# Optimization experiments

Measured on AMD Instinct MI355X. Metric: run time of the kernel, lower is better.

## Reference

```python
import jax, jax.numpy as jnp
import numpy as np

H = 768   # config.hidden_size
B = 1024  # batch
S = 256   # attention context length
C1, C2, C3 = 202, 183, 11  # num_class for crit, law, time


def setup_inputs() -> dict:
    key = jax.random.key(0)
    ks = jax.random.split(key, 18)
    sd = 1.0 / np.sqrt(H)
    def u(k, shape):
        return jax.random.uniform(k, shape, jnp.float32, -sd, sd)
    return {
        "x": jax.random.normal(ks[0], (B, H), jnp.float32),
        "attn": jax.random.normal(ks[1], (B, S, H), jnp.float32),
        # 3 LSTMCells (tasks crit, law, time), stacked
        "Wih": u(ks[2], (3, 4 * H, H)),
        "Whh": u(ks[3], (3, 4 * H, H)),
        "bih": u(ks[4], (3, 4 * H)),
        "bhh": u(ks[5], (3, 4 * H)),
        # edge (2->3) hidden/cell state Linear (only edge whose FC is reached)
        "hfc_W": u(ks[6], (H, H)), "hfc_b": u(ks[7], (H,)),
        "cfc_W": u(ks[8], (H, H)), "cfc_b": u(ks[9], (H,)),
        # midfc per task
        "midfc_W": u(ks[10], (3, H, H)), "midfc_b": u(ks[11], (3, H)),
        # outfc per task (distinct class counts)
        "out1_W": u(ks[12], (C1, H)), "out1_b": u(ks[13], (C1,)),
        "out2_W": u(ks[14], (C2, H)), "out2_b": u(ks[15], (C2,)),
        "out3_W": u(ks[16], (C3, H)), "out3_b": u(ks[17], (C3,)),
    }


def _lstm_cell(x, h, c, Wih, Whh, bih, bhh):
    # torch nn.LSTMCell: gate order i, f, g, o
    gates = x @ Wih.T + bih + h @ Whh.T + bhh
    i, f, g, o = jnp.split(gates, 4, axis=-1)
    c_new = jax.nn.sigmoid(f) * c + jax.nn.sigmoid(i) * jnp.tanh(g)
    h_new = jax.nn.sigmoid(o) * jnp.tanh(c_new)
    return h_new, c_new


def _attend(h, attn):
    # Attention: ratio = softmax(bmm(attn, h)); result = bmm(attn^T, ratio)
    w = jax.nn.softmax(jnp.einsum('bsh,bh->bs', attn, h), axis=1)
    return jnp.einsum('bsh,bs->bh', attn, w)


def _head(h, mW, mb, oW, ob):
    # more_fc=True: outfc(relu(midfc(h)))
    return jax.nn.relu(h @ mW.T + mb) @ oW.T + ob


def reference(x, attn, Wih, Whh, bih, bhh, hfc_W, hfc_b, cfc_W, cfc_b,
              midfc_W, midfc_b, out1_W, out1_b, out2_W, out2_b, out3_W, out3_b):
    # graph "[(1 2),(1 3),(2 3)]": edges 1->2, 1->3, 2->3; initial hidden_list all zero.
    z = jnp.zeros_like(x)
    # task 1 (crit): runs on zero state; first-touch sets hidden[2]=hidden[3]=(h1,c1)
    h1, c1 = _lstm_cell(x, z, z, Wih[0], Whh[0], bih[0], bhh[0])
    # task 2 (law): state = (h1, c1)
    h2, c2 = _lstm_cell(x, h1, c1, Wih[1], Whh[1], bih[1], bhh[1])
    # edge 2->3 applies the per-edge Linear and accumulates into hidden[3]
    hp3 = h1 + h2 @ hfc_W.T + hfc_b
    cp3 = c1 + c2 @ cfc_W.T + cfc_b
    # task 3 (time)
    h3, c3 = _lstm_cell(x, hp3, cp3, Wih[2], Whh[2], bih[2], bhh[2])
    # attention over encoder context, per task head
    a1 = _attend(h1, attn)
    a2 = _attend(h2, attn)
    a3 = _attend(h3, attn)
    o1 = _head(a1, midfc_W[0], midfc_b[0], out1_W, out1_b)
    o2 = _head(a2, midfc_W[1], midfc_b[1], out2_W, out2_b)
    o3 = _head(a3, midfc_W[2], midfc_b[2], out3_W, out3_b)
    return (o1, o2, o3)
```

## Files before the change

### kernel.cpp

```cpp
#include <hip/hip_runtime.h>


typedef unsigned short u16;
typedef _Float16       f16x8 __attribute__((ext_vector_type(8)));
typedef float          f32x4 __attribute__((ext_vector_type(4)));

#define SWZ(r) ((((r) + ((r) >> 2))) & 3)
#define VMCNT(N) asm volatile("s_waitcnt vmcnt(" #N ")" ::: "memory")
#define KBAR()  do { __builtin_amdgcn_s_barrier(); __builtin_amdgcn_sched_barrier(0); } while (0)

__device__ __forceinline__ u16 f2h(float f) {
  _Float16 h = (_Float16)f;
  return __builtin_bit_cast(u16, h);
}
__device__ __forceinline__ float sigm(float x) { return 1.f / (1.f + __expf(-x)); }
__device__ __forceinline__ float ftanh(float x) { return 1.f - 2.f / (__expf(2.f * x) + 1.f); }

__device__ __forceinline__ void gld16(const u16* g, u16* l) {
  __builtin_amdgcn_global_load_lds(
      (const __attribute__((address_space(1))) unsigned int*)(g),
      (__attribute__((address_space(3))) unsigned int*)(l),
      16, 0, 0);
}

struct KP { const u16 *pA, *pW0, *pW1; };

__device__ __forceinline__ void stage_tile(const KP& kp, int kt,
                                           u16* Asb, u16* Bsb, int wv) {
  const int off = kt * 32;
  gld16(kp.pA  + off, Asb + wv * 512);
  gld16(kp.pW0 + off, Bsb + wv * 512);
  gld16(kp.pW1 + off, Bsb + 2048 + wv * 512);
}

__device__ __forceinline__ void compute_tile(const u16* Asb, const u16* Bsb,
                                             int wv, int frow, int fsl, f32x4* acc) {
  const int ar = wv * 16 + frow;
  f16x8 ah = *(const f16x8*)(Asb + ar * 32 + ((fsl ^ SWZ(ar)) * 8));
  f16x8 bh[8];
#pragma unroll
  for (int n = 0; n < 8; ++n) {
    const int br = n * 16 + frow;
    bh[n] = *(const f16x8*)(Bsb + br * 32 + ((fsl ^ SWZ(br)) * 8));
  }
#pragma unroll
  for (int n = 0; n < 8; ++n)
    acc[n] = __builtin_amdgcn_mfma_f32_16x16x32_f16(ah, bh[n], acc[n], 0, 0, 0);
}

__device__ __forceinline__ void kloop(const KP& kp, u16* As, u16* Bs,
                                      int wv, int frow, int fsl, f32x4* acc) {
  const int NT = 24;
  stage_tile(kp, 0, As,        Bs,        wv);
  stage_tile(kp, 1, As + 2048, Bs + 4096, wv);
  stage_tile(kp, 2, As + 4096, Bs + 8192, wv);
  for (int t = 0; t < NT - 2; ++t) {
    VMCNT(6); KBAR();
    const int cb = t & 3;
    compute_tile(As + cb * 2048, Bs + cb * 4096, wv, frow, fsl, acc);
    if (t + 3 < NT) {
      const int sb = (t + 3) & 3;
      stage_tile(kp, t + 3, As + sb * 2048, Bs + sb * 4096, wv);
    }
  }
  VMCNT(3); KBAR();
  compute_tile(As + ((NT - 2) & 3) * 2048, Bs + ((NT - 2) & 3) * 4096,
               wv, frow, fsl, acc);
  VMCNT(0); KBAR();
  compute_tile(As + ((NT - 1) & 3) * 2048, Bs + ((NT - 1) & 3) * 4096,
               wv, frow, fsl, acc);
}

struct GJob {
  const u16* A; const u16* W;
  float* outf; u16* outh;
  const float* bias; const float* bias2; const float* addend;
  int N; int ldc; int relu;
};

__device__ __forceinline__ void run_gemm(const GJob& jb, int bx, int by,
                                         u16* As, u16* Bs, int tid) {
  const int bn0 = bx * 128;
  if (bn0 >= jb.N) return;
  const int bm0 = by * 64;
  const int lane = tid & 63, wv = tid >> 6;
  const int frow = lane & 15, fsl = lane >> 4;

  const int ra  = tid >> 2,        csa  = (tid & 3) ^ SWZ(ra);
  const int rb1 = (tid >> 2) + 64, csb1 = (tid & 3) ^ SWZ(rb1);
  int wr0 = bn0 + ra;  if (wr0 >= jb.N) wr0 = jb.N - 1;
  int wr1 = bn0 + rb1; if (wr1 >= jb.N) wr1 = jb.N - 1;

  KP kp;
  kp.pA  = jb.A + (size_t)(bm0 + ra) * 768 + csa * 8;
  kp.pW0 = jb.W + (size_t)wr0 * 768 + csa * 8;
  kp.pW1 = jb.W + (size_t)wr1 * 768 + csb1 * 8;

  f32x4 acc[8];
#pragma unroll
  for (int n = 0; n < 8; ++n) acc[n] = (f32x4){0.f, 0.f, 0.f, 0.f};

  kloop(kp, As, Bs, wv, frow, fsl, acc);

  const int rb = (lane >> 4) * 4;
  const int cc = lane & 15;
#pragma unroll
  for (int n = 0; n < 8; ++n) {
    const int col = bn0 + n * 16 + cc;
    if (col >= jb.N) continue;
    float bv = 0.f;
    if (jb.bias)  bv += jb.bias[col];
    if (jb.bias2) bv += jb.bias2[col];
    const int row0 = bm0 + wv * 16 + rb;
#pragma unroll
    for (int r = 0; r < 4; ++r) {
      const int row = row0 + r;
      float v = acc[n][r] + bv;
      if (jb.addend) v += jb.addend[(size_t)row * jb.ldc + col];
      if (jb.relu)   v = fmaxf(v, 0.f);
      if (jb.outf)   jb.outf[(size_t)row * jb.ldc + col] = v;
      if (jb.outh)   jb.outh[(size_t)row * jb.ldc + col] = f2h(v);
    }
  }
}

__device__ __forceinline__ void run_cell(const u16* A, const u16* W,
                                         const float* bi, const float* bh_,
                                         const float* addend,
                                         const float* cprev,
                                         float* hf, float* cf, u16* hh, u16* ch,
                                         int bx, int by,
                                         u16* As, u16* Bs, int tid) {
  const int bj0 = bx * 32;
  const int bm0 = by * 64;
  const int lane = tid & 63, wv = tid >> 6;
  const int frow = lane & 15, fsl = lane >> 4;

  const int ra  = tid >> 2,        csa  = (tid & 3) ^ SWZ(ra);
  const int rb1 = (tid >> 2) + 64, csb1 = (tid & 3) ^ SWZ(rb1);
  const int wr0 = (ra >> 5) * 768 + bj0 + (ra & 31);
  const int wr1 = (rb1 >> 5) * 768 + bj0 + (rb1 & 31);

  KP kp;
  kp.pA  = A + (size_t)(bm0 + ra) * 768 + csa * 8;
  kp.pW0 = W + (size_t)wr0 * 768 + csa * 8;
  kp.pW1 = W + (size_t)wr1 * 768 + csb1 * 8;

  f32x4 acc[8];
#pragma unroll
  for (int n = 0; n < 8; ++n) acc[n] = (f32x4){0.f, 0.f, 0.f, 0.f};

  kloop(kp, As, Bs, wv, frow, fsl, acc);

  const int rb = (lane >> 4) * 4;
  const int cc = lane & 15;
#pragma unroll
  for (int jj = 0; jj < 2; ++jj) {
    const int j = bj0 + jj * 16 + cc;
    float b_i = 0.f, b_f = 0.f, b_g = 0.f, b_o = 0.f;
    if (bi) {
      b_i = bi[j]        + bh_[j];
      b_f = bi[768 + j]  + bh_[768 + j];
      b_g = bi[1536 + j] + bh_[1536 + j];
      b_o = bi[2304 + j] + bh_[2304 + j];
    }
    const int row0 = bm0 + wv * 16 + rb;
#pragma unroll
    for (int r = 0; r < 4; ++r) {
      const int row = row0 + r;
      float gi = acc[0 + jj][r] + b_i;
      float gf = acc[2 + jj][r] + b_f;
      float gg = acc[4 + jj][r] + b_g;
      float go = acc[6 + jj][r] + b_o;
      if (addend) {
        const float* ad = addend + (size_t)row * 6144;
        gi += ad[j]; gf += ad[768 + j]; gg += ad[1536 + j]; go += ad[2304 + j];
      }
      float c = sigm(gi) * ftanh(gg);
      if (cprev) c += sigm(gf) * cprev[row * 768 + j];
      float h = sigm(go) * ftanh(c);
      if (hf) hf[row * 768 + j] = h;
      if (cf) cf[row * 768 + j] = c;
      if (hh) hh[row * 768 + j] = f2h(h);
      if (ch) ch[row * 768 + j] = f2h(c);
    }
  }
}

__device__ __forceinline__ void cvt_seg(const float* s, u16* d, int n4,
                                        int gtid, int nthr) {
  for (int i = gtid; i < n4; i += nthr) {
    float4 v = ((const float4*)s)[i];
    ushort4 h;
    h.x = f2h(v.x); h.y = f2h(v.y); h.z = f2h(v.z); h.w = f2h(v.w);
    ((ushort4*)d)[i] = h;
  }
}

__global__ __launch_bounds__(256)
void cvt0_k(const float* x, u16* xh, const float* Wih, u16* Wihh)
{
  const int g = blockIdx.x * 256 + threadIdx.x, N = 2048 * 256;
  cvt_seg(x,   xh,   196608,  g, N);
  cvt_seg(Wih, Wihh, 1769472, g, N);
}

struct K1P {
  const u16 *xh, *Wihh;
  const float *bih, *bhh;
  float *h1f, *c1f; u16* h1h;
  float* Gpre;
  const float *Whh, *hfcW, *cfcW, *midW, *o1W, *o2W, *o3W;
  u16 *Whhh, *hfch, *cfch, *midh, *o1h, *o2h, *o3h;
};

__global__ __launch_bounds__(256)
void k1_k(K1P p)
{
  __shared__ __align__(16) u16 As[4 * 64 * 32];
  __shared__ __align__(16) u16 Bs[4 * 128 * 32];
  const int blk = blockIdx.x, tid = threadIdx.x;

  if (blk < 384) {
    run_cell(p.xh, p.Wihh, p.bih, p.bhh, nullptr, nullptr,
             p.h1f, p.c1f, p.h1h, nullptr, blk % 24, blk / 24, As, Bs, tid);
  } else if (blk < 1152) {
    const int r = blk - 384;
    GJob jb = { p.xh, p.Wihh + (size_t)3072 * 768, p.Gpre, nullptr,
                p.bih + 3072, p.bhh + 3072, nullptr, 6144, 6144, 0 };
    run_gemm(jb, r % 48, r / 48, As, Bs, tid);
  } else {
    const int g = (blk - 1152) * 256 + tid, N = 384 * 256;
    cvt_seg(p.Whh + 2359296, p.Whhh, 1179648, g, N);
    cvt_seg(p.hfcW, p.hfch, 147456, g, N);
    cvt_seg(p.cfcW, p.cfch, 147456, g, N);
    cvt_seg(p.midW, p.midh, 442368, g, N);
    cvt_seg(p.o1W,  p.o1h,  38784,  g, N);
    cvt_seg(p.o2W,  p.o2h,  35136,  g, N);
    cvt_seg(p.o3W,  p.o3h,  2112,   g, N);
  }
}

__global__ __launch_bounds__(256)
void cell_k(const u16* __restrict__ A, const u16* __restrict__ W,
            const float* __restrict__ addend, const float* __restrict__ cprev,
            float* hf, float* cf, u16* hh, u16* ch)
{
  __shared__ __align__(16) u16 As[4 * 64 * 32];
  __shared__ __align__(16) u16 Bs[4 * 128 * 32];
  run_cell(A, W, nullptr, nullptr, addend, cprev, hf, cf, hh, ch,
           blockIdx.x, blockIdx.y, As, Bs, threadIdx.x);
}

struct GArgs { GJob j[3]; };

__global__ __launch_bounds__(256)
void gemm_k(GArgs P)
{
  __shared__ __align__(16) u16 As[4 * 64 * 32];
  __shared__ __align__(16) u16 Bs[4 * 128 * 32];
  run_gemm(P.j[blockIdx.z], blockIdx.x, blockIdx.y, As, Bs, threadIdx.x);
}

__global__ __launch_bounds__(256)
void attn_k(const float* __restrict__ attn,
            const float* __restrict__ h1, const float* __restrict__ h2,
            const float* __restrict__ h3,
            u16* __restrict__ a1, u16* __restrict__ a2, u16* __restrict__ a3)
{
  const int b = blockIdx.x, tid = threadIdx.x;
  const int lane = tid & 63, wv = tid >> 6;
  __shared__ float accW[4][3][768];
  __shared__ float lsumW[4][3];

  const float* ab = attn + (size_t)b * 196608;
  const int cb = lane * 4;

  float4 hh[3][3];
#pragma unroll
  for (int j = 0; j < 3; ++j) {
    hh[0][j] = *(const float4*)(h1 + b * 768 + j * 256 + cb);
    hh[1][j] = *(const float4*)(h2 + b * 768 + j * 256 + cb);
    hh[2][j] = *(const float4*)(h3 + b * 768 + j * 256 + cb);
  }

  float4 acc[3][3];
#pragma unroll
  for (int t3 = 0; t3 < 3; ++t3)
#pragma unroll
    for (int j = 0; j < 3; ++j) acc[t3][j] = (float4){0.f, 0.f, 0.f, 0.f};
  float lsum[3] = {0.f, 0.f, 0.f};

  const int row0 = wv * 64;
  for (int sub = 0; sub < 16; ++sub) {
    const float* rp = ab + (size_t)(row0 + sub * 4) * 768 + cb;
    float4 vv[4][3];
#pragma unroll
    for (int s = 0; s < 4; ++s)
#pragma unroll
      for (int j = 0; j < 3; ++j)
        vv[s][j] = *(const float4*)(rp + s * 768 + j * 256);

    float q[3][4];
#pragma unroll
    for (int t3 = 0; t3 < 3; ++t3)
#pragma unroll
      for (int s = 0; s < 4; ++s) {
        float d = 0.f;
#pragma unroll
        for (int j = 0; j < 3; ++j) {
          d = fmaf(vv[s][j].x, hh[t3][j].x, d);
          d = fmaf(vv[s][j].y, hh[t3][j].y, d);
          d = fmaf(vv[s][j].z, hh[t3][j].z, d);
          d = fmaf(vv[s][j].w, hh[t3][j].w, d);
        }
        q[t3][s] = d;
      }
#pragma unroll
    for (int t3 = 0; t3 < 3; ++t3)
#pragma unroll
      for (int s = 0; s < 4; ++s) {
#pragma unroll
        for (int d = 1; d < 64; d <<= 1)
          q[t3][s] += __shfl_xor(q[t3][s], d);
        q[t3][s] = __expf(q[t3][s]);
      }
#pragma unroll
    for (int t3 = 0; t3 < 3; ++t3)
#pragma unroll
      for (int s = 0; s < 4; ++s) {
        const float pw = q[t3][s];
        lsum[t3] += pw;
#pragma unroll
        for (int j = 0; j < 3; ++j) {
          acc[t3][j].x = fmaf(pw, vv[s][j].x, acc[t3][j].x);
          acc[t3][j].y = fmaf(pw, vv[s][j].y, acc[t3][j].y);
          acc[t3][j].z = fmaf(pw, vv[s][j].z, acc[t3][j].z);
          acc[t3][j].w = fmaf(pw, vv[s][j].w, acc[t3][j].w);
        }
      }
  }

#pragma unroll
  for (int t3 = 0; t3 < 3; ++t3)
#pragma unroll
    for (int j = 0; j < 3; ++j)
      *(float4*)(&accW[wv][t3][j * 256 + cb]) = acc[t3][j];
  if (lane == 0) {
#pragma unroll
    for (int t3 = 0; t3 < 3; ++t3) lsumW[wv][t3] = lsum[t3];
  }
  __syncthreads();

  float ltot[3];
#pragma unroll
  for (int t3 = 0; t3 < 3; ++t3)
    ltot[t3] = lsumW[0][t3] + lsumW[1][t3] + lsumW[2][t3] + lsumW[3][t3];
  u16* outs[3] = { a1, a2, a3 };
#pragma unroll
  for (int cc = 0; cc < 3; ++cc) {
    const int c = tid + cc * 256;
#pragma unroll
    for (int t3 = 0; t3 < 3; ++t3) {
      float s = accW[0][t3][c] + accW[1][t3][c] + accW[2][t3][c] + accW[3][t3][c];
      outs[t3][b * 768 + c] = f2h(s / ltot[t3]);
    }
  }
}

extern "C" void kernel_launch(void* const* d_in, const int* in_sizes, int n_in,
                              void* d_out, int out_size, void* d_ws, size_t ws_size,
                              hipStream_t stream)
{
  const float* x    = (const float*)d_in[0];
  const float* attn = (const float*)d_in[1];
  const float* Wih  = (const float*)d_in[2];
  const float* Whh  = (const float*)d_in[3];
  const float* bih  = (const float*)d_in[4];
  const float* bhh  = (const float*)d_in[5];
  const float* hfcW = (const float*)d_in[6];
  const float* hfcb = (const float*)d_in[7];
  const float* cfcW = (const float*)d_in[8];
  const float* cfcb = (const float*)d_in[9];
  const float* midW = (const float*)d_in[10];
  const float* midb = (const float*)d_in[11];
  const float* o1W  = (const float*)d_in[12];
  const float* o1b  = (const float*)d_in[13];
  const float* o2W  = (const float*)d_in[14];
  const float* o2b  = (const float*)d_in[15];
  const float* o3W  = (const float*)d_in[16];
  const float* o3b  = (const float*)d_in[17];
  float* out = (float*)d_out;
  char*  ws  = (char*)d_ws;

  float* Gpre = (float*)(ws + 0);
  float* h1f  = (float*)(ws + 25165824);
  float* c1f  = (float*)(ws + 28311552);
  float* h2f  = (float*)(ws + 31457280);
  float* cp3f = (float*)(ws + 34603008);
  float* h3f  = (float*)(ws + 37748736);
  u16*   xh   = (u16*)(ws + 40894464);
  u16*   Wihh = (u16*)(ws + 42467328);
  u16*   Whhh = (u16*)(ws + 56623104);
  u16*   hfch = (u16*)(ws + 66060288);
  u16*   cfch = (u16*)(ws + 67239936);
  u16*   midh = (u16*)(ws + 68419584);
  u16*   o1h  = (u16*)(ws + 71958528);
  u16*   o2h  = (u16*)(ws + 72268800);
  u16*   o3h  = (u16*)(ws + 72549888);
  u16*   h1h  = (u16*)(ws + 72566784);
  u16*   h2h  = (u16*)(ws + 74139648);
  u16*   c2h  = (u16*)(ws + 75712512);
  u16*   hp3h = (u16*)(ws + 77285376);
  u16*   a1h  = (u16*)(ws + 78858240);
  u16*   a2h  = (u16*)(ws + 80431104);
  u16*   a3h  = (u16*)(ws + 82003968);
  u16*   m1h  = (u16*)(ws + 83576832);
  u16*   m2h  = (u16*)(ws + 85149696);
  u16*   m3h  = (u16*)(ws + 86722560);

  cvt0_k<<<2048, 256, 0, stream>>>(x, xh, Wih, Wihh);

  K1P p1;
  p1.xh = xh; p1.Wihh = Wihh; p1.bih = bih; p1.bhh = bhh;
  p1.h1f = h1f; p1.c1f = c1f; p1.h1h = h1h; p1.Gpre = Gpre;
  p1.Whh = Whh; p1.hfcW = hfcW; p1.cfcW = cfcW; p1.midW = midW;
  p1.o1W = o1W; p1.o2W = o2W; p1.o3W = o3W;
  p1.Whhh = Whhh; p1.hfch = hfch; p1.cfch = cfch; p1.midh = midh;
  p1.o1h = o1h; p1.o2h = o2h; p1.o3h = o3h;
  k1_k<<<1536, 256, 0, stream>>>(p1);

  cell_k<<<dim3(24, 16), 256, 0, stream>>>(h1h, Whhh, Gpre, c1f,
                                           h2f, nullptr, h2h, c2h);

  GArgs P;
  P = GArgs{};
  P.j[0] = { h2h, hfch, nullptr, hp3h, hfcb, nullptr, h1f, 768, 768, 0 };
  P.j[1] = { c2h, cfch, cp3f, nullptr, cfcb, nullptr, c1f, 768, 768, 0 };
  P.j[2] = P.j[1];
  gemm_k<<<dim3(6, 16, 2), 256, 0, stream>>>(P);

  cell_k<<<dim3(24, 16), 256, 0, stream>>>(hp3h, Whhh + 2359296, Gpre + 3072,
                                           cp3f, h3f, nullptr, nullptr, nullptr);

  attn_k<<<1024, 256, 0, stream>>>(attn, h1f, h2f, h3f, a1h, a2h, a3h);

  P = GArgs{};
  P.j[0] = { a1h, midh,           nullptr, m1h, midb,        nullptr, nullptr, 768, 768, 1 };
  P.j[1] = { a2h, midh +  589824, nullptr, m2h, midb +  768, nullptr, nullptr, 768, 768, 1 };
  P.j[2] = { a3h, midh + 1179648, nullptr, m3h, midb + 1536, nullptr, nullptr, 768, 768, 1 };
  gemm_k<<<dim3(6, 16, 3), 256, 0, stream>>>(P);

  P = GArgs{};
  P.j[0] = { m1h, o1h, out,          nullptr, o1b, nullptr, nullptr, 202, 202, 0 };
  P.j[1] = { m2h, o2h, out + 206848, nullptr, o2b, nullptr, nullptr, 183, 183, 0 };
  P.j[2] = { m3h, o3h, out + 394240, nullptr, o3b, nullptr, nullptr,  11,  11, 0 };
  gemm_k<<<dim3(2, 16, 3), 256, 0, stream>>>(P);

  (void)in_sizes; (void)n_in; (void)out_size; (void)ws_size;
}
```

Measured before the change: 318.6 us.

## Fold hfc Linear into task-3 LSTM weights and fuse edge GEMMs into cell3

Rewrites task 3's recurrent term algebraically: hp3 @ Whh3^T becomes h1 @ Whh3^T + h2 @ (Whh3·hfcW)^T + Whh3·hfc_b. The combined weight W2 and bias b3 are precomputed inside k1 alongside other weight work. The new cell3 kernel runs a 48-tile K loop over two A/W pairs and computes the cfc GEMM for cp3 inline, so the separate edge gemm launch and its hp3/cp3 round-trips go away. In exchange it adds a 768x768x3072 weight GEMM and a strided transpose of hfcW per call, doubles the K loop in the cell kernel, and rounds the fused weight to fp16.

```diff
diff --git a/kernel.cpp b/kernel.cpp
--- a/kernel.cpp
+++ b/kernel.cpp
@@ -23,14 +23,15 @@
       16, 0, 0);
 }
 
-struct KP { const u16 *pA, *pW0, *pW1; };
-
-__device__ __forceinline__ void stage_tile(const KP& kp, int kt,
+struct KP { const u16 *pA1, *pA2, *pW1_0, *pW2_0, *pW1_1, *pW2_1; };
+
+__device__ __forceinline__ void stage_tile(const KP& kp, int kt, int ntA,
                                            u16* Asb, u16* Bsb, int wv) {
-  const int off = kt * 32;
-  gld16(kp.pA  + off, Asb + wv * 512);
-  gld16(kp.pW0 + off, Bsb + wv * 512);
-  gld16(kp.pW1 + off, Bsb + 2048 + wv * 512);
+  const bool s1 = (kt < ntA);
+  const int off = (s1 ? kt : kt - ntA) * 32;
+  gld16((s1 ? kp.pA1   : kp.pA2  ) + off, Asb + wv * 512);
+  gld16((s1 ? kp.pW1_0 : kp.pW2_0) + off, Bsb + wv * 512);
+  gld16((s1 ? kp.pW1_1 : kp.pW2_1) + off, Bsb + 2048 + wv * 512);
 }
 
 __device__ __forceinline__ void compute_tile(const u16* Asb, const u16* Bsb,
@@ -48,19 +49,19 @@
     acc[n] = __builtin_amdgcn_mfma_f32_16x16x32_f16(ah, bh[n], acc[n], 0, 0, 0);
 }
 
-__device__ __forceinline__ void kloop(const KP& kp, u16* As, u16* Bs,
-                                      int wv, int frow, int fsl, f32x4* acc) {
-  const int NT = 24;
-  stage_tile(kp, 0, As,        Bs,        wv);
-  stage_tile(kp, 1, As + 2048, Bs + 4096, wv);
-  stage_tile(kp, 2, As + 4096, Bs + 8192, wv);
+__device__ __forceinline__ void kloop4(const KP& kp, int ntA, int NT,
+                                       u16* As, u16* Bs,
+                                       int wv, int frow, int fsl, f32x4* acc) {
+  stage_tile(kp, 0, ntA, As,        Bs,        wv);
+  stage_tile(kp, 1, ntA, As + 2048, Bs + 4096, wv);
+  stage_tile(kp, 2, ntA, As + 4096, Bs + 8192, wv);
   for (int t = 0; t < NT - 2; ++t) {
     VMCNT(6); KBAR();
     const int cb = t & 3;
     compute_tile(As + cb * 2048, Bs + cb * 4096, wv, frow, fsl, acc);
     if (t + 3 < NT) {
       const int sb = (t + 3) & 3;
-      stage_tile(kp, t + 3, As + sb * 2048, Bs + sb * 4096, wv);
+      stage_tile(kp, t + 3, ntA, As + sb * 2048, Bs + sb * 4096, wv);
     }
   }
   VMCNT(3); KBAR();
@@ -92,15 +93,15 @@
   int wr1 = bn0 + rb1; if (wr1 >= jb.N) wr1 = jb.N - 1;
 
   KP kp;
-  kp.pA  = jb.A + (size_t)(bm0 + ra) * 768 + csa * 8;
-  kp.pW0 = jb.W + (size_t)wr0 * 768 + csa * 8;
-  kp.pW1 = jb.W + (size_t)wr1 * 768 + csb1 * 8;
+  kp.pA1 = kp.pA2 = jb.A + (size_t)(bm0 + ra) * 768 + csa * 8;
+  kp.pW1_0 = kp.pW2_0 = jb.W + (size_t)wr0 * 768 + csa * 8;
+  kp.pW1_1 = kp.pW2_1 = jb.W + (size_t)wr1 * 768 + csb1 * 8;
 
   f32x4 acc[8];
 #pragma unroll
   for (int n = 0; n < 8; ++n) acc[n] = (f32x4){0.f, 0.f, 0.f, 0.f};
 
-  kloop(kp, As, Bs, wv, frow, fsl, acc);
+  kloop4(kp, 24, 24, As, Bs, wv, frow, fsl, acc);
 
   const int rb = (lane >> 4) * 4;
   const int cc = lane & 15;
@@ -142,15 +143,15 @@
   const int wr1 = (rb1 >> 5) * 768 + bj0 + (rb1 & 31);
 
   KP kp;
-  kp.pA  = A + (size_t)(bm0 + ra) * 768 + csa * 8;
-  kp.pW0 = W + (size_t)wr0 * 768 + csa * 8;
-  kp.pW1 = W + (size_t)wr1 * 768 + csb1 * 8;
+  kp.pA1 = kp.pA2 = A + (size_t)(bm0 + ra) * 768 + csa * 8;
+  kp.pW1_0 = kp.pW2_0 = W + (size_t)wr0 * 768 + csa * 8;
+  kp.pW1_1 = kp.pW2_1 = W + (size_t)wr1 * 768 + csb1 * 8;
 
   f32x4 acc[8];
 #pragma unroll
   for (int n = 0; n < 8; ++n) acc[n] = (f32x4){0.f, 0.f, 0.f, 0.f};
 
-  kloop(kp, As, Bs, wv, frow, fsl, acc);
+  kloop4(kp, 24, 24, As, Bs, wv, frow, fsl, acc);
 
   const int rb = (lane >> 4) * 4;
   const int cc = lane & 15;
@@ -198,20 +199,26 @@
 }
 
 __global__ __launch_bounds__(256)
-void cvt0_k(const float* x, u16* xh, const float* Wih, u16* Wihh)
+void cvt0_k(const float* x, u16* xh, const float* Wih, u16* Wihh,
+            const float* Whh3, u16* Whh3h, const float* hfcW, u16* hfcTh)
 {
   const int g = blockIdx.x * 256 + threadIdx.x, N = 2048 * 256;
-  cvt_seg(x,   xh,   196608,  g, N);
-  cvt_seg(Wih, Wihh, 1769472, g, N);
+  cvt_seg(x,    xh,    196608,  g, N);
+  cvt_seg(Wih,  Wihh,  1769472, g, N);
+  cvt_seg(Whh3, Whh3h, 589824,  g, N);
+  for (int i = g; i < 589824; i += N) {
+    const int k = i / 768, m = i - k * 768;
+    hfcTh[i] = f2h(hfcW[m * 768 + k]);
+  }
 }
 
 struct K1P {
-  const u16 *xh, *Wihh;
-  const float *bih, *bhh;
-  float *h1f, *c1f; u16* h1h;
-  float* Gpre;
-  const float *Whh, *hfcW, *cfcW, *midW, *o1W, *o2W, *o3W;
-  u16 *Whhh, *hfch, *cfch, *midh, *o1h, *o2h, *o3h;
+  const u16 *xh, *Wihh, *Whh3h, *hfcTh;
+  const float *bih, *bhh, *Whh, *hfcb;
+  float *h1f, *c1f, *b3f, *Gpre;
+  u16 *h1h, *W2h;
+  const float *cfcW, *midW, *o1W, *o2W, *o3W;
+  u16 *Whh1h, *cfch, *midh, *o1h, *o2h, *o3h;
 };
 
 __global__ __launch_bounds__(256)
@@ -229,10 +236,24 @@
     GJob jb = { p.xh, p.Wihh + (size_t)3072 * 768, p.Gpre, nullptr,
                 p.bih + 3072, p.bhh + 3072, nullptr, 6144, 6144, 0 };
     run_gemm(jb, r % 48, r / 48, As, Bs, tid);
+  } else if (blk < 1440) {
+    const int r = blk - 1152;
+    GJob jb = { p.Whh3h, p.hfcTh, nullptr, p.W2h,
+                nullptr, nullptr, nullptr, 768, 768, 0 };
+    run_gemm(jb, r % 6, r / 6, As, Bs, tid);
+  } else if (blk < 1452) {
+    const int g = (blk - 1440) * 256 + tid;
+    const float* wrow = p.Whh + 4718592 + (size_t)g * 768;
+    float s = 0.f;
+    for (int m = 0; m < 768; m += 4) {
+      float4 wv4 = *(const float4*)(wrow + m);
+      float4 bv4 = *(const float4*)(p.hfcb + m);
+      s += wv4.x * bv4.x + wv4.y * bv4.y + wv4.z * bv4.z + wv4.w * bv4.w;
+    }
+    p.b3f[g] = s;
   } else {
-    const int g = (blk - 1152) * 256 + tid, N = 384 * 256;
-    cvt_seg(p.Whh + 2359296, p.Whhh, 1179648, g, N);
-    cvt_seg(p.hfcW, p.hfch, 147456, g, N);
+    const int g = (blk - 1452) * 256 + tid, N = 84 * 256;
+    cvt_seg(p.Whh + 2359296, p.Whh1h, 589824, g, N);
     cvt_seg(p.cfcW, p.cfch, 147456, g, N);
     cvt_seg(p.midW, p.midh, 442368, g, N);
     cvt_seg(p.o1W,  p.o1h,  38784,  g, N);
@@ -242,14 +263,112 @@
 }
 
 __global__ __launch_bounds__(256)
-void cell_k(const u16* __restrict__ A, const u16* __restrict__ W,
-            const float* __restrict__ addend, const float* __restrict__ cprev,
-            float* hf, float* cf, u16* hh, u16* ch)
+void cell2_k(const u16* __restrict__ A, const u16* __restrict__ W,
+             const float* __restrict__ addend, const float* __restrict__ cprev,
+             float* hf, u16* hh, u16* ch)
 {
   __shared__ __align__(16) u16 As[4 * 64 * 32];
   __shared__ __align__(16) u16 Bs[4 * 128 * 32];
-  run_cell(A, W, nullptr, nullptr, addend, cprev, hf, cf, hh, ch,
+  run_cell(A, W, nullptr, nullptr, addend, cprev, hf, nullptr, hh, ch,
            blockIdx.x, blockIdx.y, As, Bs, threadIdx.x);
+}
+
+__global__ __launch_bounds__(256)
+void cell3_k(const u16* __restrict__ h1h, const u16* __restrict__ h2h,
+             const u16* __restrict__ c2h,
+             const u16* __restrict__ Whh3h, const u16* __restrict__ W2h,
+             const u16* __restrict__ cfch,
+             const float* __restrict__ b3f, const float* __restrict__ Gpre3,
+             const float* __restrict__ c1f, const float* __restrict__ cfcb,
+             float* __restrict__ h3f)
+{
+  __shared__ __align__(16) u16 As[4 * 64 * 32];
+  __shared__ __align__(16) u16 Bs[4 * 128 * 32];
+  const int bj0 = blockIdx.x * 32;
+  const int bm0 = blockIdx.y * 64;
+  const int tid = threadIdx.x, lane = tid & 63, wv = tid >> 6;
+  const int frow = lane & 15, fsl = lane >> 4;
+
+  const int ra  = tid >> 2,        csa  = (tid & 3) ^ SWZ(ra);
+  const int rb1 = (tid >> 2) + 64, csb1 = (tid & 3) ^ SWZ(rb1);
+  const int wr0 = (ra >> 5) * 768 + bj0 + (ra & 31);
+  const int wr1 = (rb1 >> 5) * 768 + bj0 + (rb1 & 31);
+
+  KP kp;
+  kp.pA1   = h1h + (size_t)(bm0 + ra) * 768 + csa * 8;
+  kp.pA2   = h2h + (size_t)(bm0 + ra) * 768 + csa * 8;
+  kp.pW1_0 = Whh3h + (size_t)wr0 * 768 + csa * 8;
+  kp.pW2_0 = W2h   + (size_t)wr0 * 768 + csa * 8;
+  kp.pW1_1 = Whh3h + (size_t)wr1 * 768 + csb1 * 8;
+  kp.pW2_1 = W2h   + (size_t)wr1 * 768 + csb1 * 8;
+
+  f32x4 acc[8];
+#pragma unroll
+  for (int n = 0; n < 8; ++n) acc[n] = (f32x4){0.f, 0.f, 0.f, 0.f};
+
+  kloop4(kp, 24, 48, As, Bs, wv, frow, fsl, acc);
+
+  const int qb = tid & 127;
+  const int rc = qb >> 2, csc = (qb & 3) ^ SWZ(rc);
+  const u16* pA3 = c2h  + (size_t)(bm0 + ra) * 768 + csa * 8;
+  const u16* pC  = cfch + (size_t)(bj0 + rc) * 768 + csc * 8;
+  const int bdst = (wv < 2) ? wv * 512 : 1024 + wv * 512;
+
+  f32x4 accc[2];
+  accc[0] = (f32x4){0.f, 0.f, 0.f, 0.f};
+  accc[1] = (f32x4){0.f, 0.f, 0.f, 0.f};
+
+#define MSTAGE(t) do { const int mb_ = (t) & 3;                         \
+    gld16(pA3 + (t) * 32, As + mb_ * 2048 + wv * 512);                  \
+    gld16(pC  + (t) * 32, Bs + mb_ * 4096 + bdst); } while (0)
+#define MCOMP(t) do { const int mb_ = (t) & 3;                          \
+    const u16* Ab_ = As + mb_ * 2048; const u16* Bb_ = Bs + mb_ * 4096; \
+    const int ar_ = wv * 16 + frow;                                     \
+    f16x8 ah_ = *(const f16x8*)(Ab_ + ar_ * 32 + ((fsl ^ SWZ(ar_)) * 8)); \
+    const int b0_ = frow, b1_ = 16 + frow;                              \
+    f16x8 f0_ = *(const f16x8*)(Bb_ + b0_ * 32 + ((fsl ^ SWZ(b0_)) * 8)); \
+    f16x8 f1_ = *(const f16x8*)(Bb_ + b1_ * 32 + ((fsl ^ SWZ(b1_)) * 8)); \
+    accc[0] = __builtin_amdgcn_mfma_f32_16x16x32_f16(ah_, f0_, accc[0], 0, 0, 0); \
+    accc[1] = __builtin_amdgcn_mfma_f32_16x16x32_f16(ah_, f1_, accc[1], 0, 0, 0); \
+  } while (0)
+
+  MSTAGE(0); MSTAGE(1); MSTAGE(2);
+  for (int t = 0; t < 22; ++t) {
+    VMCNT(4); KBAR();
+    MCOMP(t);
+    if (t + 3 < 24) MSTAGE(t + 3);
+  }
+  VMCNT(2); KBAR();
+  MCOMP(22);
+  VMCNT(0); KBAR();
+  MCOMP(23);
+#undef MSTAGE
+#undef MCOMP
+
+  const int rb = (lane >> 4) * 4;
+  const int cc = lane & 15;
+#pragma unroll
+  for (int jj = 0; jj < 2; ++jj) {
+    const int j = bj0 + jj * 16 + cc;
+    const float b_i = b3f[j];
+    const float b_f = b3f[768 + j];
+    const float b_g = b3f[1536 + j];
+    const float b_o = b3f[2304 + j];
+    const float cb_ = cfcb[j];
+    const int row0 = bm0 + wv * 16 + rb;
+#pragma unroll
+    for (int r = 0; r < 4; ++r) {
+      const int row = row0 + r;
+      const float* ad = Gpre3 + (size_t)row * 6144;
+      float gi = acc[0 + jj][r] + b_i + ad[j];
+      float gf = acc[2 + jj][r] + b_f + ad[768 + j];
+      float gg = acc[4 + jj][r] + b_g + ad[1536 + j];
+      float go = acc[6 + jj][r] + b_o + ad[2304 + j];
+      float cp3 = accc[jj][r] + c1f[row * 768 + j] + cb_;
+      float c = sigm(gf) * cp3 + sigm(gi) * ftanh(gg);
+      h3f[row * 768 + j] = sigm(go) * ftanh(c);
+    }
+  }
 }
 
 struct GArgs { GJob j[3]; };
@@ -393,58 +512,56 @@
   float* out = (float*)d_out;
   char*  ws  = (char*)d_ws;
 
-  float* Gpre = (float*)(ws + 0);
-  float* h1f  = (float*)(ws + 25165824);
-  float* c1f  = (float*)(ws + 28311552);
-  float* h2f  = (float*)(ws + 31457280);
-  float* cp3f = (float*)(ws + 34603008);
-  float* h3f  = (float*)(ws + 37748736);
-  u16*   xh   = (u16*)(ws + 40894464);
-  u16*   Wihh = (u16*)(ws + 42467328);
-  u16*   Whhh = (u16*)(ws + 56623104);
-  u16*   hfch = (u16*)(ws + 66060288);
-  u16*   cfch = (u16*)(ws + 67239936);
-  u16*   midh = (u16*)(ws + 68419584);
-  u16*   o1h  = (u16*)(ws + 71958528);
-  u16*   o2h  = (u16*)(ws + 72268800);
-  u16*   o3h  = (u16*)(ws + 72549888);
-  u16*   h1h  = (u16*)(ws + 72566784);
-  u16*   h2h  = (u16*)(ws + 74139648);
-  u16*   c2h  = (u16*)(ws + 75712512);
-  u16*   hp3h = (u16*)(ws + 77285376);
-  u16*   a1h  = (u16*)(ws + 78858240);
-  u16*   a2h  = (u16*)(ws + 80431104);
-  u16*   a3h  = (u16*)(ws + 82003968);
-  u16*   m1h  = (u16*)(ws + 83576832);
-  u16*   m2h  = (u16*)(ws + 85149696);
-  u16*   m3h  = (u16*)(ws + 86722560);
-
-  cvt0_k<<<2048, 256, 0, stream>>>(x, xh, Wih, Wihh);
+  float* Gpre  = (float*)(ws + 0);
+  float* h1f   = (float*)(ws + 25165824);
+  float* c1f   = (float*)(ws + 28311552);
+  float* h2f   = (float*)(ws + 31457280);
+  float* h3f   = (float*)(ws + 34603008);
+  float* b3f   = (float*)(ws + 37748736);
+  u16*   xh    = (u16*)(ws + 37765120);
+  u16*   Wihh  = (u16*)(ws + 39337984);
+  u16*   Whh1h = (u16*)(ws + 53493760);
+  u16*   Whh3h = (u16*)(ws + 58212352);
+  u16*   hfcTh = (u16*)(ws + 62930944);
+  u16*   W2h   = (u16*)(ws + 64110592);
+  u16*   cfch  = (u16*)(ws + 68829184);
+  u16*   midh  = (u16*)(ws + 70008832);
+  u16*   o1h   = (u16*)(ws + 73547776);
+  u16*   o2h   = (u16*)(ws + 73858048);
+  u16*   o3h   = (u16*)(ws + 74139648);
+  u16*   h1h   = (u16*)(ws + 74157056);
+  u16*   h2h   = (u16*)(ws + 75729920);
+  u16*   c2h   = (u16*)(ws + 77302784);
+  u16*   a1h   = (u16*)(ws + 78875648);
+  u16*   a2h   = (u16*)(ws + 80448512);
+  u16*   a3h   = (u16*)(ws + 82021376);
+  u16*   m1h   = (u16*)(ws + 83594240);
+  u16*   m2h   = (u16*)(ws + 85167104);
+  u16*   m3h   = (u16*)(ws + 86739968);
+
+  cvt0_k<<<2048, 256, 0, stream>>>(x, xh, Wih, Wihh,
+                                   Whh + 4718592, Whh3h, hfcW, hfcTh);
 
   K1P p1;
-  p1.xh = xh; p1.Wihh = Wihh; p1.bih = bih; p1.bhh = bhh;
-  p1.h1f = h1f; p1.c1f = c1f; p1.h1h = h1h; p1.Gpre = Gpre;
-  p1.Whh = Whh; p1.hfcW = hfcW; p1.cfcW = cfcW; p1.midW = midW;
+  p1.xh = xh; p1.Wihh = Wihh; p1.Whh3h = Whh3h; p1.hfcTh = hfcTh;
+  p1.bih = bih; p1.bhh = bhh; p1.Whh = Whh; p1.hfcb = hfcb;
+  p1.h1f = h1f; p1.c1f = c1f; p1.b3f = b3f; p1.Gpre = Gpre;
+  p1.h1h = h1h; p1.W2h = W2h;
+  p1.cfcW = cfcW; p1.midW = midW;
   p1.o1W = o1W; p1.o2W = o2W; p1.o3W = o3W;
-  p1.Whhh = Whhh; p1.hfch = hfch; p1.cfch = cfch; p1.midh = midh;
+  p1.Whh1h = Whh1h; p1.cfch = cfch; p1.midh = midh;
   p1.o1h = o1h; p1.o2h = o2h; p1.o3h = o3h;
   k1_k<<<1536, 256, 0, stream>>>(p1);
 
-  cell_k<<<dim3(24, 16), 256, 0, stream>>>(h1h, Whhh, Gpre, c1f,
-                                           h2f, nullptr, h2h, c2h);
+  cell2_k<<<dim3(24, 16), 256, 0, stream>>>(h1h, Whh1h, Gpre, c1f,
+                                            h2f, h2h, c2h);
+
+  cell3_k<<<dim3(24, 16), 256, 0, stream>>>(h1h, h2h, c2h, Whh3h, W2h, cfch,
+                                            b3f, Gpre + 3072, c1f, cfcb, h3f);
+
+  attn_k<<<1024, 256, 0, stream>>>(attn, h1f, h2f, h3f, a1h, a2h, a3h);
 
   GArgs P;
-  P = GArgs{};
-  P.j[0] = { h2h, hfch, nullptr, hp3h, hfcb, nullptr, h1f, 768, 768, 0 };
-  P.j[1] = { c2h, cfch, cp3f, nullptr, cfcb, nullptr, c1f, 768, 768, 0 };
-  P.j[2] = P.j[1];
-  gemm_k<<<dim3(6, 16, 2), 256, 0, stream>>>(P);
-
-  cell_k<<<dim3(24, 16), 256, 0, stream>>>(hp3h, Whhh + 2359296, Gpre + 3072,
-                                           cp3f, h3f, nullptr, nullptr, nullptr);
-
-  attn_k<<<1024, 256, 0, stream>>>(attn, h1f, h2f, h3f, a1h, a2h, a3h);
-
   P = GArgs{};
   P.j[0] = { a1h, midh,           nullptr, m1h, midb,        nullptr, nullptr, 768, 768, 1 };
   P.j[1] = { a2h, midh +  589824, nullptr, m2h, midb +  768, nullptr, nullptr, 768, 768, 1 };
```

Result: slower. 350.0 us (median of 2 runs) (+9.9%).

## Halve GEMM/cell tiles to 64 columns and move task-3 precompute into cell-2 kernel

Applied to the files above, without the earlier changes.

Adds 64x64 tile variants of the GEMM and fused LSTM-cell paths (16 hidden units per block), which doubles the block count for the small 1024-row GEMMs so more CUs are busy. The task-3 input-gate precompute (x@Wih3) is moved out of k1 into the new k2 kernel, where it runs alongside the task-2 recurrent cell. This balances work across the two launches. Smaller tiles reduce per-block data reuse and increase weight-load traffic relative to MFMA work.

```diff
diff --git a/kernel.cpp b/kernel.cpp
--- a/kernel.cpp
+++ b/kernel.cpp
@@ -48,9 +48,8 @@
     acc[n] = __builtin_amdgcn_mfma_f32_16x16x32_f16(ah, bh[n], acc[n], 0, 0, 0);
 }
 
-__device__ __forceinline__ void kloop(const KP& kp, u16* As, u16* Bs,
-                                      int wv, int frow, int fsl, f32x4* acc) {
-  const int NT = 24;
+__device__ __forceinline__ void kloop4(const KP& kp, int NT, u16* As, u16* Bs,
+                                       int wv, int frow, int fsl, f32x4* acc) {
   stage_tile(kp, 0, As,        Bs,        wv);
   stage_tile(kp, 1, As + 2048, Bs + 4096, wv);
   stage_tile(kp, 2, As + 4096, Bs + 8192, wv);
@@ -78,8 +77,8 @@
   int N; int ldc; int relu;
 };
 
-__device__ __forceinline__ void run_gemm(const GJob& jb, int bx, int by,
-                                         u16* As, u16* Bs, int tid) {
+__device__ __forceinline__ void run_gemm128(const GJob& jb, int bx, int by,
+                                            u16* As, u16* Bs, int tid) {
   const int bn0 = bx * 128;
   if (bn0 >= jb.N) return;
   const int bm0 = by * 64;
@@ -100,7 +99,7 @@
 #pragma unroll
   for (int n = 0; n < 8; ++n) acc[n] = (f32x4){0.f, 0.f, 0.f, 0.f};
 
-  kloop(kp, As, Bs, wv, frow, fsl, acc);
+  kloop4(kp, 24, As, Bs, wv, frow, fsl, acc);
 
   const int rb = (lane >> 4) * 4;
   const int cc = lane & 15;
@@ -124,66 +123,149 @@
   }
 }
 
-__device__ __forceinline__ void run_cell(const u16* A, const u16* W,
-                                         const float* bi, const float* bh_,
-                                         const float* addend,
-                                         const float* cprev,
-                                         float* hf, float* cf, u16* hh, u16* ch,
-                                         int bx, int by,
-                                         u16* As, u16* Bs, int tid) {
-  const int bj0 = bx * 32;
+struct KP64 { const u16 *pA, *pW; };
+
+__device__ __forceinline__ void stage64(const KP64& kp, int kt,
+                                        u16* Asb, u16* Bsb, int wv) {
+  const int off = kt * 32;
+  gld16(kp.pA + off, Asb + wv * 512);
+  gld16(kp.pW + off, Bsb + wv * 512);
+}
+
+__device__ __forceinline__ void compute64(const u16* Asb, const u16* Bsb,
+                                          int wv, int frow, int fsl, f32x4* acc) {
+  const int ar = wv * 16 + frow;
+  f16x8 ah = *(const f16x8*)(Asb + ar * 32 + ((fsl ^ SWZ(ar)) * 8));
+  f16x8 bh[4];
+#pragma unroll
+  for (int n = 0; n < 4; ++n) {
+    const int br = n * 16 + frow;
+    bh[n] = *(const f16x8*)(Bsb + br * 32 + ((fsl ^ SWZ(br)) * 8));
+  }
+#pragma unroll
+  for (int n = 0; n < 4; ++n)
+    acc[n] = __builtin_amdgcn_mfma_f32_16x16x32_f16(ah, bh[n], acc[n], 0, 0, 0);
+}
+
+__device__ __forceinline__ void kloop64(const KP64& kp, int NT, u16* As, u16* Bs,
+                                        int wv, int frow, int fsl, f32x4* acc) {
+  stage64(kp, 0, As,        Bs,        wv);
+  stage64(kp, 1, As + 2048, Bs + 2048, wv);
+  stage64(kp, 2, As + 4096, Bs + 4096, wv);
+  for (int t = 0; t < NT - 2; ++t) {
+    VMCNT(4); KBAR();
+    const int cb = t & 3;
+    compute64(As + cb * 2048, Bs + cb * 2048, wv, frow, fsl, acc);
+    if (t + 3 < NT) {
+      const int sb = (t + 3) & 3;
+      stage64(kp, t + 3, As + sb * 2048, Bs + sb * 2048, wv);
+    }
+  }
+  VMCNT(2); KBAR();
+  compute64(As + ((NT - 2) & 3) * 2048, Bs + ((NT - 2) & 3) * 2048,
+            wv, frow, fsl, acc);
+  VMCNT(0); KBAR();
+  compute64(As + ((NT - 1) & 3) * 2048, Bs + ((NT - 1) & 3) * 2048,
+            wv, frow, fsl, acc);
+}
+
+__device__ __forceinline__ void run_gemm64(const GJob& jb, int bx, int by,
+                                           u16* As, u16* Bs, int tid) {
+  const int bn0 = bx * 64;
+  if (bn0 >= jb.N) return;
   const int bm0 = by * 64;
   const int lane = tid & 63, wv = tid >> 6;
   const int frow = lane & 15, fsl = lane >> 4;
 
-  const int ra  = tid >> 2,        csa  = (tid & 3) ^ SWZ(ra);
-  const int rb1 = (tid >> 2) + 64, csb1 = (tid & 3) ^ SWZ(rb1);
-  const int wr0 = (ra >> 5) * 768 + bj0 + (ra & 31);
-  const int wr1 = (rb1 >> 5) * 768 + bj0 + (rb1 & 31);
-
-  KP kp;
-  kp.pA  = A + (size_t)(bm0 + ra) * 768 + csa * 8;
-  kp.pW0 = W + (size_t)wr0 * 768 + csa * 8;
-  kp.pW1 = W + (size_t)wr1 * 768 + csb1 * 8;
-
-  f32x4 acc[8];
-#pragma unroll
-  for (int n = 0; n < 8; ++n) acc[n] = (f32x4){0.f, 0.f, 0.f, 0.f};
-
-  kloop(kp, As, Bs, wv, frow, fsl, acc);
+  const int ra = tid >> 2, csa = (tid & 3) ^ SWZ(ra);
+  int wr = bn0 + ra; if (wr >= jb.N) wr = jb.N - 1;
+
+  KP64 kp;
+  kp.pA = jb.A + (size_t)(bm0 + ra) * 768 + csa * 8;
+  kp.pW = jb.W + (size_t)wr * 768 + csa * 8;
+
+  f32x4 acc[4];
+#pragma unroll
+  for (int n = 0; n < 4; ++n) acc[n] = (f32x4){0.f, 0.f, 0.f, 0.f};
+
+  kloop64(kp, 24, As, Bs, wv, frow, fsl, acc);
 
   const int rb = (lane >> 4) * 4;
   const int cc = lane & 15;
 #pragma unroll
-  for (int jj = 0; jj < 2; ++jj) {
-    const int j = bj0 + jj * 16 + cc;
-    float b_i = 0.f, b_f = 0.f, b_g = 0.f, b_o = 0.f;
-    if (bi) {
-      b_i = bi[j]        + bh_[j];
-      b_f = bi[768 + j]  + bh_[768 + j];
-      b_g = bi[1536 + j] + bh_[1536 + j];
-      b_o = bi[2304 + j] + bh_[2304 + j];
-    }
+  for (int n = 0; n < 4; ++n) {
+    const int col = bn0 + n * 16 + cc;
+    if (col >= jb.N) continue;
+    float bv = 0.f;
+    if (jb.bias)  bv += jb.bias[col];
+    if (jb.bias2) bv += jb.bias2[col];
     const int row0 = bm0 + wv * 16 + rb;
 #pragma unroll
     for (int r = 0; r < 4; ++r) {
       const int row = row0 + r;
-      float gi = acc[0 + jj][r] + b_i;
-      float gf = acc[2 + jj][r] + b_f;
-      float gg = acc[4 + jj][r] + b_g;
-      float go = acc[6 + jj][r] + b_o;
-      if (addend) {
-        const float* ad = addend + (size_t)row * 6144;
-        gi += ad[j]; gf += ad[768 + j]; gg += ad[1536 + j]; go += ad[2304 + j];
-      }
-      float c = sigm(gi) * ftanh(gg);
-      if (cprev) c += sigm(gf) * cprev[row * 768 + j];
-      float h = sigm(go) * ftanh(c);
-      if (hf) hf[row * 768 + j] = h;
-      if (cf) cf[row * 768 + j] = c;
-      if (hh) hh[row * 768 + j] = f2h(h);
-      if (ch) ch[row * 768 + j] = f2h(c);
+      float v = acc[n][r] + bv;
+      if (jb.addend) v += jb.addend[(size_t)row * jb.ldc + col];
+      if (jb.relu)   v = fmaxf(v, 0.f);
+      if (jb.outf)   jb.outf[(size_t)row * jb.ldc + col] = v;
+      if (jb.outh)   jb.outh[(size_t)row * jb.ldc + col] = f2h(v);
     }
+  }
+}
+
+__device__ __forceinline__ void run_cell64(const u16* A, const u16* W,
+                                           const float* bi, const float* bh_,
+                                           const float* addend,
+                                           const float* cprev,
+                                           float* hf, float* cf, u16* hh, u16* ch,
+                                           int bx, int by,
+                                           u16* As, u16* Bs, int tid) {
+  const int bj0 = bx * 16;
+  const int bm0 = by * 64;
+  const int lane = tid & 63, wv = tid >> 6;
+  const int frow = lane & 15, fsl = lane >> 4;
+
+  const int ra = tid >> 2, csa = (tid & 3) ^ SWZ(ra);
+  const int wr = (ra >> 4) * 768 + bj0 + (ra & 15);
+
+  KP64 kp;
+  kp.pA = A + (size_t)(bm0 + ra) * 768 + csa * 8;
+  kp.pW = W + (size_t)wr * 768 + csa * 8;
+
+  f32x4 acc[4];
+#pragma unroll
+  for (int n = 0; n < 4; ++n) acc[n] = (f32x4){0.f, 0.f, 0.f, 0.f};
+
+  kloop64(kp, 24, As, Bs, wv, frow, fsl, acc);
+
+  const int rb = (lane >> 4) * 4;
+  const int cc = lane & 15;
+  const int j = bj0 + cc;
+  float b_i = 0.f, b_f = 0.f, b_g = 0.f, b_o = 0.f;
+  if (bi) {
+    b_i = bi[j]        + bh_[j];
+    b_f = bi[768 + j]  + bh_[768 + j];
+    b_g = bi[1536 + j] + bh_[1536 + j];
+    b_o = bi[2304 + j] + bh_[2304 + j];
+  }
+  const int row0 = bm0 + wv * 16 + rb;
+#pragma unroll
+  for (int r = 0; r < 4; ++r) {
+    const int row = row0 + r;
+    float gi = acc[0][r] + b_i;
+    float gf = acc[1][r] + b_f;
+    float gg = acc[2][r] + b_g;
+    float go = acc[3][r] + b_o;
+    if (addend) {
+      const float* ad = addend + (size_t)row * 6144;
+      gi += ad[j]; gf += ad[768 + j]; gg += ad[1536 + j]; go += ad[2304 + j];
+    }
+    float c = sigm(gi) * ftanh(gg);
+    if (cprev) c += sigm(gf) * cprev[row * 768 + j];
+    float h = sigm(go) * ftanh(c);
+    if (hf) hf[row * 768 + j] = h;
+    if (cf) cf[row * 768 + j] = c;
+    if (hh) hh[row * 768 + j] = f2h(h);
+    if (ch) ch[row * 768 + j] = f2h(c);
   }
 }
 
@@ -217,18 +299,18 @@
 __global__ __launch_bounds__(256)
 void k1_k(K1P p)
 {
-  __shared__ __align__(16) u16 As[4 * 64 * 32];
-  __shared__ __align__(16) u16 Bs[4 * 128 * 32];
+  __shared__ __align__(16) u16 As[8192];
+  __shared__ __align__(16) u16 Bs[16384];
   const int blk = blockIdx.x, tid = threadIdx.x;
 
-  if (blk < 384) {
-    run_cell(p.xh, p.Wihh, p.bih, p.bhh, nullptr, nullptr,
-             p.h1f, p.c1f, p.h1h, nullptr, blk % 24, blk / 24, As, Bs, tid);
+  if (blk < 768) {
+    run_cell64(p.xh, p.Wihh, p.bih, p.bhh, nullptr, nullptr,
+               p.h1f, p.c1f, p.h1h, nullptr, blk % 48, blk / 48, As, Bs, tid);
   } else if (blk < 1152) {
-    const int r = blk - 384;
+    const int r = blk - 768;
     GJob jb = { p.xh, p.Wihh + (size_t)3072 * 768, p.Gpre, nullptr,
-                p.bih + 3072, p.bhh + 3072, nullptr, 6144, 6144, 0 };
-    run_gemm(jb, r % 48, r / 48, As, Bs, tid);
+                p.bih + 3072, p.bhh + 3072, nullptr, 3072, 6144, 0 };
+    run_gemm128(jb, r % 24, r / 24, As, Bs, tid);
   } else {
     const int g = (blk - 1152) * 256 + tid, N = 384 * 256;
     cvt_seg(p.Whh + 2359296, p.Whhh, 1179648, g, N);
@@ -241,25 +323,49 @@
   }
 }
 
+struct K2P {
+  const u16 *h1h, *Whhh, *xh, *Wihh;
+  const float *Gpre_t2, *c1f, *bih, *bhh;
+  float *h2f, *Gpre_t3; u16 *h2h, *c2h;
+};
+
 __global__ __launch_bounds__(256)
-void cell_k(const u16* __restrict__ A, const u16* __restrict__ W,
-            const float* __restrict__ addend, const float* __restrict__ cprev,
-            float* hf, float* cf, u16* hh, u16* ch)
-{
-  __shared__ __align__(16) u16 As[4 * 64 * 32];
-  __shared__ __align__(16) u16 Bs[4 * 128 * 32];
-  run_cell(A, W, nullptr, nullptr, addend, cprev, hf, cf, hh, ch,
-           blockIdx.x, blockIdx.y, As, Bs, threadIdx.x);
+void k2_k(K2P p)
+{
+  __shared__ __align__(16) u16 As[8192];
+  __shared__ __align__(16) u16 Bs[16384];
+  const int blk = blockIdx.x, tid = threadIdx.x;
+
+  if (blk < 768) {
+    run_cell64(p.h1h, p.Whhh, nullptr, nullptr, p.Gpre_t2, p.c1f,
+               p.h2f, nullptr, p.h2h, p.c2h, blk % 48, blk / 48, As, Bs, tid);
+  } else {
+    const int r = blk - 768;
+    GJob jb = { p.xh, p.Wihh + (size_t)6144 * 768, p.Gpre_t3, nullptr,
+                p.bih + 6144, p.bhh + 6144, nullptr, 3072, 6144, 0 };
+    run_gemm128(jb, r % 24, r / 24, As, Bs, tid);
+  }
+}
+
+__global__ __launch_bounds__(256)
+void cell3_k(const u16* __restrict__ A, const u16* __restrict__ W,
+             const float* __restrict__ addend, const float* __restrict__ cprev,
+             float* hf)
+{
+  __shared__ __align__(16) u16 As[8192];
+  __shared__ __align__(16) u16 Bs[8192];
+  run_cell64(A, W, nullptr, nullptr, addend, cprev, hf, nullptr, nullptr, nullptr,
+             blockIdx.x, blockIdx.y, As, Bs, threadIdx.x);
 }
 
 struct GArgs { GJob j[3]; };
 
 __global__ __launch_bounds__(256)
-void gemm_k(GArgs P)
-{
-  __shared__ __align__(16) u16 As[4 * 64 * 32];
-  __shared__ __align__(16) u16 Bs[4 * 128 * 32];
-  run_gemm(P.j[blockIdx.z], blockIdx.x, blockIdx.y, As, Bs, threadIdx.x);
+void gemm64_k(GArgs P)
+{
+  __shared__ __align__(16) u16 As[8192];
+  __shared__ __align__(16) u16 Bs[8192];
+  run_gemm64(P.j[blockIdx.z], blockIdx.x, blockIdx.y, As, Bs, threadIdx.x);
 }
 
 __global__ __launch_bounds__(256)
@@ -430,18 +536,21 @@
   p1.o1h = o1h; p1.o2h = o2h; p1.o3h = o3h;
   k1_k<<<1536, 256, 0, stream>>>(p1);
 
-  cell_k<<<dim3(24, 16), 256, 0, stream>>>(h1h, Whhh, Gpre, c1f,
-                                           h2f, nullptr, h2h, c2h);
+  K2P p2;
+  p2.h1h = h1h; p2.Whhh = Whhh; p2.xh = xh; p2.Wihh = Wihh;
+  p2.Gpre_t2 = Gpre; p2.c1f = c1f; p2.bih = bih; p2.bhh = bhh;
+  p2.h2f = h2f; p2.Gpre_t3 = Gpre + 3072; p2.h2h = h2h; p2.c2h = c2h;
+  k2_k<<<1152, 256, 0, stream>>>(p2);
 
   GArgs P;
   P = GArgs{};
   P.j[0] = { h2h, hfch, nullptr, hp3h, hfcb, nullptr, h1f, 768, 768, 0 };
   P.j[1] = { c2h, cfch, cp3f, nullptr, cfcb, nullptr, c1f, 768, 768, 0 };
   P.j[2] = P.j[1];
-  gemm_k<<<dim3(6, 16, 2), 256, 0, stream>>>(P);
-
-  cell_k<<<dim3(24, 16), 256, 0, stream>>>(hp3h, Whhh + 2359296, Gpre + 3072,
-                                           cp3f, h3f, nullptr, nullptr, nullptr);
+  gemm64_k<<<dim3(12, 16, 2), 256, 0, stream>>>(P);
+
+  cell3_k<<<dim3(48, 16), 256, 0, stream>>>(hp3h, Whhh + 2359296,
+                                            Gpre + 3072, cp3f, h3f);
 
   attn_k<<<1024, 256, 0, stream>>>(attn, h1f, h2f, h3f, a1h, a2h, a3h);
 
@@ -449,13 +558,13 @@
   P.j[0] = { a1h, midh,           nullptr, m1h, midb,        nullptr, nullptr, 768, 768, 1 };
   P.j[1] = { a2h, midh +  589824, nullptr, m2h, midb +  768, nullptr, nullptr, 768, 768, 1 };
   P.j[2] = { a3h, midh + 1179648, nullptr, m3h, midb + 1536, nullptr, nullptr, 768, 768, 1 };
-  gemm_k<<<dim3(6, 16, 3), 256, 0, stream>>>(P);
+  gemm64_k<<<dim3(12, 16, 3), 256, 0, stream>>>(P);
 
   P = GArgs{};
   P.j[0] = { m1h, o1h, out,          nullptr, o1b, nullptr, nullptr, 202, 202, 0 };
   P.j[1] = { m2h, o2h, out + 206848, nullptr, o2b, nullptr, nullptr, 183, 183, 0 };
   P.j[2] = { m3h, o3h, out + 394240, nullptr, o3b, nullptr, nullptr,  11,  11, 0 };
-  gemm_k<<<dim3(2, 16, 3), 256, 0, stream>>>(P);
+  gemm64_k<<<dim3(4, 16, 3), 256, 0, stream>>>(P);
 
   (void)in_sizes; (void)n_in; (void)out_size; (void)ws_size;
 }
```

After: 309.0 us. -3.0%, faster.
